# Optimization experiments

Hardware: AMD Instinct MI355X
Metric: run time of the kernel (lower is better)

## Reference

```python
import jax, jax.numpy as jnp
import numpy as np

WS = 7            # window size per spatial dim
NW = WS ** 3      # tokens per window = 343
EPS = 1e-5


def _rel_pos_index():
    # MONAI 3D relative position index, shape (NW, NW), values in [0, 13^3)
    coords = np.stack(np.meshgrid(np.arange(WS), np.arange(WS), np.arange(WS), indexing='ij'))
    cf = coords.reshape(3, -1)                       # (3, NW)
    rel = (cf[:, :, None] - cf[:, None, :]).transpose(1, 2, 0).astype(np.int64)  # (NW, NW, 3)
    rel += WS - 1
    rel[:, :, 0] *= (2 * WS - 1) * (2 * WS - 1)
    rel[:, :, 1] *= (2 * WS - 1)
    return rel.sum(-1)

_RPI = _rel_pos_index()


def layer_norm(x, g, b):
    mu = jnp.mean(x, axis=-1, keepdims=True)
    var = jnp.mean(jnp.square(x - mu), axis=-1, keepdims=True)
    return (x - mu) * jax.lax.rsqrt(var + EPS) * g + b


def _forward(x, pe_w, pe_bias, pe_g, pe_b, n1_g, n1_b, qkv_w, rpb, proj_w, proj_b,
             n2_g, n2_b, fc1_w, fc1_b, fc2_w, fc2_b):
    # ---- PatchEmbed: Conv3d stride=patch + LayerNorm over channel ----
    h = jax.lax.conv_general_dilated(x, pe_w, (2, 2, 2), 'VALID',
                                     dimension_numbers=('NCDHW', 'OIDHW', 'NCDHW'))
    h = h + pe_bias[None, :, None, None, None]
    b, c, d, hh, w = h.shape
    t = h.reshape(b, c, -1).transpose(0, 2, 1)       # (b, d*h*w, c)
    t = layer_norm(t, pe_g, pe_b)
    h = t.transpose(0, 2, 1).reshape(b, c, d, hh, w)
    # dropout(p=0) and proj_out(normalize=False) are identity

    xe = h.transpose(0, 2, 3, 4, 1)                  # (b, d, h, w, c)
    rpi = jnp.asarray(_RPI)
    num_heads = rpb.shape[-1]
    hd = c // num_heads
    scale = hd ** -0.5
    nd, nh_, nw_ = d // WS, hh // WS, w // WS        # window grid (7,7,7)

    for i in range(qkv_w.shape[0]):                  # 3 Swin blocks, all shift=0
        shortcut = xe
        y = layer_norm(xe, n1_g[i], n1_b[i])
        # window partition -> (b*nW, NW, c)
        yw = y.reshape(b, nd, WS, nh_, WS, nw_, WS, c)
        yw = yw.transpose(0, 1, 3, 5, 2, 4, 6, 7).reshape(-1, NW, c)
        # windowed MSA with relative position bias (qkv_bias=False)
        qkv = (yw @ qkv_w[i].T).reshape(-1, NW, 3, num_heads, hd).transpose(2, 0, 3, 1, 4)
        q, k, v = qkv[0] * scale, qkv[1], qkv[2]     # (Bw, nh, NW, hd)
        attn = jnp.einsum('bhnd,bhmd->bhnm', q, k)
        bias = rpb[i][rpi].transpose(2, 0, 1)        # (nh, NW, NW)
        attn = jax.nn.softmax(attn + bias[None], axis=-1)
        o = jnp.einsum('bhnm,bhmd->bhnd', attn, v)
        o = o.transpose(0, 2, 1, 3).reshape(-1, NW, c)
        o = o @ proj_w[i].T + proj_b[i]
        # window reverse
        o = o.reshape(b, nd, nh_, nw_, WS, WS, WS, c)
        o = o.transpose(0, 1, 4, 2, 5, 3, 6, 7).reshape(b, d, hh, w, c)
        xe = shortcut + o
        # MLP (GELU exact, mlp_ratio=4)
        z = layer_norm(xe, n2_g[i], n2_b[i])
        z = jax.nn.gelu(z @ fc1_w[i].T + fc1_b[i], approximate=False)
        xe = xe + (z @ fc2_w[i].T + fc2_b[i])

    return xe.transpose(0, 4, 1, 2, 3)               # (b, c, d, h, w)


def setup_inputs() -> dict:
    key = jax.random.key(0)
    ks = jax.random.split(key, 16)
    C, NH, NB, MLP = 16, 2, 3, 64
    s = 0.02
    return {
        'x': jax.random.normal(ks[0], (1, 1, 98, 98, 98), jnp.float32),
        'pe_w': jax.random.normal(ks[1], (C, 1, 2, 2, 2), jnp.float32) * s,
        'pe_bias': jnp.zeros((C,), jnp.float32),
        'pe_g': jnp.ones((C,), jnp.float32),
        'pe_b': jnp.zeros((C,), jnp.float32),
        'n1_g': jnp.ones((NB, C), jnp.float32),
        'n1_b': jnp.zeros((NB, C), jnp.float32),
        'qkv_w': jax.random.normal(ks[2], (NB, 3 * C, C), jnp.float32) * s,
        'rpb': jax.random.normal(ks[3], (NB, (2 * WS - 1) ** 3, NH), jnp.float32) * s,
        'proj_w': jax.random.normal(ks[4], (NB, C, C), jnp.float32) * s,
        'proj_b': jnp.zeros((NB, C), jnp.float32),
        'n2_g': jnp.ones((NB, C), jnp.float32),
        'n2_b': jnp.zeros((NB, C), jnp.float32),
        'fc1_w': jax.random.normal(ks[5], (NB, MLP, C), jnp.float32) * s,
        'fc1_b': jnp.zeros((NB, MLP), jnp.float32),
        'fc2_w': jax.random.normal(ks[6], (NB, C, MLP), jnp.float32) * s,
        'fc2_b': jnp.zeros((NB, C), jnp.float32),
    }


def reference(x, pe_w, pe_bias, pe_g, pe_b, n1_g, n1_b, qkv_w, rpb, proj_w, proj_b,
              n2_g, n2_b, fc1_w, fc1_b, fc2_w, fc2_b):
    return _forward(x, pe_w, pe_bias, pe_g, pe_b, n1_g, n1_b, qkv_w, rpb, proj_w,
                    proj_b, n2_g, n2_b, fc1_w, fc1_b, fc2_w, fc2_b)
```

## Files before the change

### kernel.cpp

```cpp
#include <hip/hip_runtime.h>
#include <math.h>

#define NWTOK 343
#define NTOK 117649
#define QSCALE 0.510069734f
#define LOG2E 1.4426950408889634f
#define QPLANE 1372
#define OPLANE 2744
#define NPAD 352
#define NTILE 22

typedef unsigned int u32;
typedef __fp16 h2 __attribute__((ext_vector_type(2)));
typedef __fp16 h4 __attribute__((ext_vector_type(4)));
typedef float f32x4 __attribute__((ext_vector_type(4)));

__device__ __forceinline__ u32 packh2(float a, float b) {
    h2 h = __builtin_amdgcn_cvt_pkrtz(a, b);
    return __builtin_bit_cast(u32, h);
}
__device__ __forceinline__ h4 packh4(float a, float b, float c, float d) {
    return __builtin_bit_cast(h4, make_uint2(packh2(a, b), packh2(c, d)));
}
__device__ __forceinline__ float fast_exp2(float x) {
#if __has_builtin(__builtin_amdgcn_exp2f)
    return __builtin_amdgcn_exp2f(x);
#else
    return exp2f(x);
#endif
}

__device__ __forceinline__ float dot16_lds(const float* __restrict__ wrow,
                                           const float* __restrict__ v) {
    const float4 w0 = *(const float4*)(wrow);
    const float4 w1 = *(const float4*)(wrow + 4);
    const float4 w2 = *(const float4*)(wrow + 8);
    const float4 w3 = *(const float4*)(wrow + 12);
    float a = v[0] * w0.x;
    a = fmaf(v[1], w0.y, a); a = fmaf(v[2], w0.z, a); a = fmaf(v[3], w0.w, a);
    a = fmaf(v[4], w1.x, a); a = fmaf(v[5], w1.y, a); a = fmaf(v[6], w1.z, a);
    a = fmaf(v[7], w1.w, a);
    a = fmaf(v[8], w2.x, a); a = fmaf(v[9], w2.y, a); a = fmaf(v[10], w2.z, a);
    a = fmaf(v[11], w2.w, a);
    a = fmaf(v[12], w3.x, a); a = fmaf(v[13], w3.y, a); a = fmaf(v[14], w3.z, a);
    a = fmaf(v[15], w3.w, a);
    return a;
}

__device__ __forceinline__ float gelu_exact(float x) {
    const float z = x * 0.70710678118654752f;
    const float az = fabsf(z);
    const float t = __builtin_amdgcn_rcpf(fmaf(0.3275911f, az, 1.0f));
    float y = fmaf(t, 1.061405429f, -1.453152027f);
    y = fmaf(t, y, 1.421413741f);
    y = fmaf(t, y, -0.284496736f);
    y = fmaf(t, y, 0.254829592f);
    y *= t;
    const float one_m_erf = y * __expf(-az * az);
    const float erf_az = 1.0f - one_m_erf;
    const float erf_z = (z < 0.f) ? -erf_az : erf_az;
    return 0.5f * x * (1.0f + erf_z);
}

__device__ __forceinline__ void store_f16_row(u32* base, int t, const float* v8) {
    uint4 u;
    u.x = packh2(v8[0], v8[1]); u.y = packh2(v8[2], v8[3]);
    u.z = packh2(v8[4], v8[5]); u.w = packh2(v8[6], v8[7]);
    *(uint4*)(base + t * 4) = u;
}

__global__ __launch_bounds__(256) void k_bias_expand(
    const float* __restrict__ rpb,
    __fp16* __restrict__ bexp16)
{
    const int tile = blockIdx.x;
    const int kt = tile % NTILE;
    const int rest = tile / NTILE;
    const int qt = rest % NTILE;
    const int bh = rest / NTILE;
    const int blk = bh >> 1, h = bh & 1;
    const int tid = threadIdx.x;
    const int n = tid >> 4, g = tid & 15;
    const int i = qt * 16 + n, j = kt * 16 + g;
    float val;
    if (j >= NWTOK) {
        val = -60.f;
    } else if (i >= NWTOK) {
        val = 0.f;
    } else {
        const int iz = i / 49, ir = i - iz * 49, iy = ir / 7, ix = ir - iy * 7;
        const int jz = j / 49, jr = j - jz * 49, jy = jr / 7, jx = jr - jy * 7;
        const int idx = (iz - jz + 6) * 169 + (iy - jy + 6) * 13 + (ix - jx + 6);
        val = rpb[((size_t)blk * 2197 + idx) * 2 + h] * LOG2E;
    }
    bexp16[(size_t)tile * 256 + tid] = (__fp16)val;
}

__global__ __launch_bounds__(256, 2) void k0_patch_qkv(
    const float* __restrict__ x,
    const float* __restrict__ pe_w,
    const float* __restrict__ pe_bias,
    const float* __restrict__ pe_g,
    const float* __restrict__ pe_b,
    const float* __restrict__ n1_g,
    const float* __restrict__ n1_b,
    const float* __restrict__ qkv_w,
    float* __restrict__ xe,
    u32* __restrict__ qg,
    u32* __restrict__ kg,
    u32* __restrict__ vg)
{
    __shared__ float w_s[128];
    __shared__ float pb_s[16], g_s[16], b_s[16], n1g_s[16], n1b_s[16];
    __shared__ float qkvw_s[768];
    const int tid = threadIdx.x;
    if (tid < 128) w_s[tid] = pe_w[tid];
    if (tid < 16) {
        pb_s[tid] = pe_bias[tid]; g_s[tid] = pe_g[tid]; b_s[tid] = pe_b[tid];
        n1g_s[tid] = n1_g[tid]; n1b_s[tid] = n1_b[tid];
    }
    for (int i = tid; i < 768; i += 256) qkvw_s[i] = qkv_w[i];
    __syncthreads();
    const int g = blockIdx.x * 256 + tid;
    if (g >= NTOK) return;
    const int z = g / 2401;
    const int r = g - z * 2401;
    const int y = r / 49;
    const int xx = r - y * 49;
    const float* bp = x + ((2 * z) * 98 + (2 * y)) * 98 + 2 * xx;
    float in[8];
    in[0] = bp[0];    in[1] = bp[1];
    in[2] = bp[98];   in[3] = bp[99];
    in[4] = bp[9604]; in[5] = bp[9605];
    in[6] = bp[9702]; in[7] = bp[9703];
    float v[16];
    float mu = 0.f;
    #pragma unroll
    for (int c = 0; c < 16; ++c) {
        float a = pb_s[c];
        #pragma unroll
        for (int k = 0; k < 8; ++k) a = fmaf(in[k], w_s[c * 8 + k], a);
        v[c] = a; mu += a;
    }
    mu *= 0.0625f;
    float var = 0.f;
    #pragma unroll
    for (int c = 0; c < 16; ++c) { float d = v[c] - mu; var = fmaf(d, d, var); }
    var *= 0.0625f;
    float rs = rsqrtf(var + 1e-5f);
    float o[16];
    #pragma unroll
    for (int c = 0; c < 16; ++c) o[c] = (v[c] - mu) * rs * g_s[c] + b_s[c];

    const int zw = z / 7, zi = z - zw * 7;
    const int yw = y / 7, yi = y - yw * 7;
    const int xw = xx / 7, xi = xx - xw * 7;
    const int w = (zw * 7 + yw) * 7 + xw;
    const int t = (zi * 7 + yi) * 7 + xi;
    const int widx = w * NWTOK + t;

    float4* dst = (float4*)(xe + (size_t)widx * 16);
    dst[0] = ((float4*)o)[0]; dst[1] = ((float4*)o)[1];
    dst[2] = ((float4*)o)[2]; dst[3] = ((float4*)o)[3];

    mu = 0.f;
    #pragma unroll
    for (int c = 0; c < 16; ++c) mu += o[c];
    mu *= 0.0625f;
    var = 0.f;
    #pragma unroll
    for (int c = 0; c < 16; ++c) { float d = o[c] - mu; var = fmaf(d, d, var); }
    var *= 0.0625f;
    rs = rsqrtf(var + 1e-5f);
    float yv[16];
    #pragma unroll
    for (int c = 0; c < 16; ++c) yv[c] = (o[c] - mu) * rs * n1g_s[c] + n1b_s[c];

    float tmp[16];
    #pragma unroll
    for (int rr = 0; rr < 16; ++rr) tmp[rr] = dot16_lds(qkvw_s + rr * 16, yv) * QSCALE;
    store_f16_row(qg + (size_t)(w * 2) * QPLANE, t, tmp);
    store_f16_row(qg + (size_t)(w * 2 + 1) * QPLANE, t, tmp + 8);
    #pragma unroll
    for (int rr = 0; rr < 16; ++rr) tmp[rr] = dot16_lds(qkvw_s + (16 + rr) * 16, yv);
    store_f16_row(kg + (size_t)(w * 2) * QPLANE, t, tmp);
    store_f16_row(kg + (size_t)(w * 2 + 1) * QPLANE, t, tmp + 8);
    #pragma unroll
    for (int rr = 0; rr < 16; ++rr) tmp[rr] = dot16_lds(qkvw_s + (32 + rr) * 16, yv);
    store_f16_row(vg + (size_t)(w * 2) * QPLANE, t, tmp);
    store_f16_row(vg + (size_t)(w * 2 + 1) * QPLANE, t, tmp + 8);
}

__global__ __launch_bounds__(704, 5) void k_attn(
    const u32* __restrict__ qg,
    const u32* __restrict__ kg,
    const u32* __restrict__ vg,
    float* __restrict__ og,
    const __fp16* __restrict__ bexp_blk)
{
    __shared__ __fp16 Kl[2][NPAD][16];
    __shared__ __fp16 Ql[2][NPAD][16];
    __shared__ __fp16 Vt[2][16][360];

    const int tid = threadIdx.x;
    const int pidx = blockIdx.x;
    const int wp = pidx >> 1;
    const int h = pidx & 1;
    const int w0 = 2 * wp;
    const int w1 = (w0 + 1 < NWTOK) ? w0 + 1 : NWTOK - 1;
    const int wh0 = w0 * 2 + h;
    const int wh1 = w1 * 2 + h;

    {
        const int sw = (tid >= NPAD) ? 1 : 0;
        const int st = tid - sw * NPAD;
        const size_t qpl = (size_t)(sw ? wh1 : wh0) * QPLANE;
        const uint4 z4 = make_uint4(0, 0, 0, 0);
        if (st < NWTOK) {
            const uint4 kw = ((const uint4*)(kg + qpl))[st];
            const uint4 qw = ((const uint4*)(qg + qpl))[st];
            const uint4 vw = ((const uint4*)(vg + qpl))[st];
            *(uint4*)&Kl[sw][st][0] = kw; *(uint4*)&Kl[sw][st][8] = z4;
            *(uint4*)&Ql[sw][st][0] = qw; *(uint4*)&Ql[sw][st][8] = z4;
            const h2 v01 = __builtin_bit_cast(h2, vw.x);
            const h2 v23 = __builtin_bit_cast(h2, vw.y);
            const h2 v45 = __builtin_bit_cast(h2, vw.z);
            const h2 v67 = __builtin_bit_cast(h2, vw.w);
            Vt[sw][0][st] = v01.x; Vt[sw][1][st] = v01.y;
            Vt[sw][2][st] = v23.x; Vt[sw][3][st] = v23.y;
            Vt[sw][4][st] = v45.x; Vt[sw][5][st] = v45.y;
            Vt[sw][6][st] = v67.x; Vt[sw][7][st] = v67.y;
        } else {
            *(uint4*)&Kl[sw][st][0] = z4; *(uint4*)&Kl[sw][st][8] = z4;
            *(uint4*)&Ql[sw][st][0] = z4; *(uint4*)&Ql[sw][st][8] = z4;
            #pragma unroll
            for (int d = 0; d < 8; ++d) Vt[sw][d][st] = (__fp16)0.f;
        }
        #pragma unroll
        for (int d = 8; d < 16; ++d) Vt[sw][d][st] = (__fp16)0.f;
    }
    __syncthreads();

    const int wave = tid >> 6;
    const int lane = tid & 63;
    const int n = lane & 15;
    const int g4 = (lane >> 4) * 4;

    const int qiA = (2 * wave) * 16 + n;
    const int qiB = qiA + 16;
    const h4 bqA0 = *(const h4*)&Ql[0][qiA][g4];
    const h4 bqB0 = *(const h4*)&Ql[0][qiB][g4];
    const h4 bqA1 = *(const h4*)&Ql[1][qiA][g4];
    const h4 bqB1 = *(const h4*)&Ql[1][qiB][g4];

    const int laneoff = n * 16 + g4;
    const __fp16* trowA = bexp_blk + ((size_t)(h * 484) + (size_t)(2 * wave) * NTILE) * 256 + laneoff;
    const __fp16* trowB = trowA + (size_t)NTILE * 256;

    f32x4 accA0 = {0.f, 0.f, 0.f, 0.f}, accB0 = {0.f, 0.f, 0.f, 0.f};
    f32x4 accA1 = {0.f, 0.f, 0.f, 0.f}, accB1 = {0.f, 0.f, 0.f, 0.f};
    float lA0 = 0.f, lB0 = 0.f, lA1 = 0.f, lB1 = 0.f;

    #pragma unroll
    for (int kt = 0; kt < NTILE; ++kt) {
        const uint2 cbA16 = *(const uint2*)(trowA + kt * 256);
        const uint2 cbB16 = *(const uint2*)(trowB + kt * 256);
        const h2 alo = __builtin_bit_cast(h2, cbA16.x);
        const h2 ahi = __builtin_bit_cast(h2, cbA16.y);
        const h2 blo = __builtin_bit_cast(h2, cbB16.x);
        const h2 bhi = __builtin_bit_cast(h2, cbB16.y);
        f32x4 cbAf, cbBf;
        cbAf[0] = (float)alo.x; cbAf[1] = (float)alo.y;
        cbAf[2] = (float)ahi.x; cbAf[3] = (float)ahi.y;
        cbBf[0] = (float)blo.x; cbBf[1] = (float)blo.y;
        cbBf[2] = (float)bhi.x; cbBf[3] = (float)bhi.y;

        const h4 ak0 = *(const h4*)&Kl[0][kt * 16 + n][g4];
        const h4 ak1 = *(const h4*)&Kl[1][kt * 16 + n][g4];
        const h4 av0 = *(const h4*)&Vt[0][n][kt * 16 + g4];
        const h4 av1 = *(const h4*)&Vt[1][n][kt * 16 + g4];

        f32x4 sA0 = __builtin_amdgcn_mfma_f32_16x16x16f16(ak0, bqA0, cbAf, 0, 0, 0);
        f32x4 sB0 = __builtin_amdgcn_mfma_f32_16x16x16f16(ak0, bqB0, cbBf, 0, 0, 0);
        f32x4 sA1 = __builtin_amdgcn_mfma_f32_16x16x16f16(ak1, bqA1, cbAf, 0, 0, 0);
        f32x4 sB1 = __builtin_amdgcn_mfma_f32_16x16x16f16(ak1, bqB1, cbBf, 0, 0, 0);

        const float pA00 = fast_exp2(sA0[0]);
        const float pA01 = fast_exp2(sA0[1]);
        const float pA02 = fast_exp2(sA0[2]);
        const float pA03 = fast_exp2(sA0[3]);
        const float pB00 = fast_exp2(sB0[0]);
        const float pB01 = fast_exp2(sB0[1]);
        const float pB02 = fast_exp2(sB0[2]);
        const float pB03 = fast_exp2(sB0[3]);
        const float pA10 = fast_exp2(sA1[0]);
        const float pA11 = fast_exp2(sA1[1]);
        const float pA12 = fast_exp2(sA1[2]);
        const float pA13 = fast_exp2(sA1[3]);
        const float pB10 = fast_exp2(sB1[0]);
        const float pB11 = fast_exp2(sB1[1]);
        const float pB12 = fast_exp2(sB1[2]);
        const float pB13 = fast_exp2(sB1[3]);

        lA0 += (pA00 + pA01) + (pA02 + pA03);
        lB0 += (pB00 + pB01) + (pB02 + pB03);
        lA1 += (pA10 + pA11) + (pA12 + pA13);
        lB1 += (pB10 + pB11) + (pB12 + pB13);

        const h4 bpA0 = packh4(pA00, pA01, pA02, pA03);
        const h4 bpB0 = packh4(pB00, pB01, pB02, pB03);
        const h4 bpA1 = packh4(pA10, pA11, pA12, pA13);
        const h4 bpB1 = packh4(pB10, pB11, pB12, pB13);

        accA0 = __builtin_amdgcn_mfma_f32_16x16x16f16(av0, bpA0, accA0, 0, 0, 0);
        accB0 = __builtin_amdgcn_mfma_f32_16x16x16f16(av0, bpB0, accB0, 0, 0, 0);
        accA1 = __builtin_amdgcn_mfma_f32_16x16x16f16(av1, bpA1, accA1, 0, 0, 0);
        accB1 = __builtin_amdgcn_mfma_f32_16x16x16f16(av1, bpB1, accB1, 0, 0, 0);
    }

    lA0 += __shfl_xor(lA0, 16); lA0 += __shfl_xor(lA0, 32);
    lB0 += __shfl_xor(lB0, 16); lB0 += __shfl_xor(lB0, 32);
    lA1 += __shfl_xor(lA1, 16); lA1 += __shfl_xor(lA1, 32);
    lB1 += __shfl_xor(lB1, 16); lB1 += __shfl_xor(lB1, 32);

    if (g4 < 8) {
        if (qiA < NWTOK) {
            const f32x4 o0 = accA0 * (1.f / lA0);
            *(f32x4*)(og + (size_t)wh0 * OPLANE + qiA * 8 + g4) = o0;
            const f32x4 o1 = accA1 * (1.f / lA1);
            *(f32x4*)(og + (size_t)wh1 * OPLANE + qiA * 8 + g4) = o1;
        }
        if (qiB < NWTOK) {
            const f32x4 o0 = accB0 * (1.f / lB0);
            *(f32x4*)(og + (size_t)wh0 * OPLANE + qiB * 8 + g4) = o0;
            const f32x4 o1 = accB1 * (1.f / lB1);
            *(f32x4*)(og + (size_t)wh1 * OPLANE + qiB * 8 + g4) = o1;
        }
    }
}

__global__ __launch_bounds__(256, 4) void k_post(
    float* __restrict__ xe,
    const float* __restrict__ og,
    u32* __restrict__ qg,
    u32* __restrict__ kg,
    u32* __restrict__ vg,
    const float* __restrict__ proj_w,
    const float* __restrict__ proj_b,
    const float* __restrict__ n2_g,
    const float* __restrict__ n2_b,
    const float* __restrict__ fc1_w,
    const float* __restrict__ fc1_b,
    const float* __restrict__ fc2_w,
    const float* __restrict__ fc2_b,
    const float* __restrict__ n1_g_nx,
    const float* __restrict__ n1_b_nx,
    const float* __restrict__ qkv_w_nx,
    float* __restrict__ outp,
    const int last)
{
    __shared__ u32 projh[128];
    __shared__ u32 fc1h[512];
    __shared__ u32 fc2h[512];
    __shared__ u32 qkvh[384];
    __shared__ float projb_s[16], n2g_s[16], n2b_s[16], fc2b_s[16], n1g_s[16], n1b_s[16];
    __shared__ float fc1b_s[64];
    const int tid = threadIdx.x;
    if (tid < 128) {
        const float2 p = ((const float2*)proj_w)[tid];
        projh[tid] = packh2(p.x, p.y);
    }
    for (int i = tid; i < 512; i += 256) {
        const float2 a = ((const float2*)fc1_w)[i];
        fc1h[i] = packh2(a.x, a.y);
        const float2 b = ((const float2*)fc2_w)[i];
        fc2h[i] = packh2(b.x, b.y);
    }
    for (int i = tid; i < 384; i += 256) {
        const float2 a = ((const float2*)qkv_w_nx)[i];
        qkvh[i] = packh2(a.x, a.y);
    }
    if (tid < 16) {
        projb_s[tid] = proj_b[tid];
        n2g_s[tid] = n2_g[tid]; n2b_s[tid] = n2_b[tid];
        fc2b_s[tid] = fc2_b[tid];
        n1g_s[tid] = n1_g_nx[tid]; n1b_s[tid] = n1_b_nx[tid];
    }
    if (tid < 64) fc1b_s[tid] = fc1_b[tid];
    __syncthreads();

    const int wave_id = blockIdx.x * 4 + (tid >> 6);
    if (wave_id >= NWTOK * NTILE) return;
    const int w = wave_id / NTILE;
    const int qt = wave_id - w * NTILE;

    const int lane = tid & 63;
    const int tcol = lane & 15;
    const int g4 = (lane >> 4) * 4;
    const int tok = qt * 16 + tcol;
    const bool valid = (tok < NWTOK);
    const int tokc = valid ? tok : (NWTOK - 1);

    const f32x4 zero = {0.f, 0.f, 0.f, 0.f};

    const int pl = g4 >> 3;
    const int po = g4 & 7;
    const float4 o4 = *(const float4*)(og + (size_t)(w * 2 + pl) * OPLANE + tokc * 8 + po);
    const h4 oB = packh4(o4.x, o4.y, o4.z, o4.w);

    const uint2 apw = *(const uint2*)(projh + tcol * 8 + (g4 >> 1));
    const f32x4 d1 = __builtin_amdgcn_mfma_f32_16x16x16f16(
        __builtin_bit_cast(h4, apw), oB, zero, 0, 0, 0);
    const float4 xe4 = *(const float4*)(xe + (size_t)(w * NWTOK + tokc) * 16 + g4);
    const float4 pb4 = *(const float4*)(projb_s + g4);
    float xr0 = d1[0] + xe4.x + pb4.x;
    float xr1 = d1[1] + xe4.y + pb4.y;
    float xr2 = d1[2] + xe4.z + pb4.z;
    float xr3 = d1[3] + xe4.w + pb4.w;

    float s = (xr0 + xr1) + (xr2 + xr3);
    s += __shfl_xor(s, 16); s += __shfl_xor(s, 32);
    float mu = s * 0.0625f;
    float v0 = xr0 - mu, v1 = xr1 - mu, v2 = xr2 - mu, v3 = xr3 - mu;
    float vv = fmaf(v0, v0, fmaf(v1, v1, fmaf(v2, v2, v3 * v3)));
    vv += __shfl_xor(vv, 16); vv += __shfl_xor(vv, 32);
    float rs = rsqrtf(vv * 0.0625f + 1e-5f);
    const float4 g2 = *(const float4*)(n2g_s + g4);
    const float4 b2 = *(const float4*)(n2b_s + g4);
    const h4 zB = packh4(v0 * rs * g2.x + b2.x, v1 * rs * g2.y + b2.y,
                         v2 * rs * g2.z + b2.z, v3 * rs * g2.w + b2.w);

    h4 hB[4];
    #pragma unroll
    for (int i = 0; i < 4; ++i) {
        const uint2 aw = *(const uint2*)(fc1h + (i * 16 + tcol) * 8 + (g4 >> 1));
        f32x4 hd = __builtin_amdgcn_mfma_f32_16x16x16f16(
            __builtin_bit_cast(h4, aw), zB, zero, 0, 0, 0);
        const float4 fb = *(const float4*)(fc1b_s + i * 16 + g4);
        hB[i] = packh4(gelu_exact(hd[0] + fb.x), gelu_exact(hd[1] + fb.y),
                       gelu_exact(hd[2] + fb.z), gelu_exact(hd[3] + fb.w));
    }

    f32x4 acc = zero;
    #pragma unroll
    for (int j = 0; j < 4; ++j) {
        const uint2 aw = *(const uint2*)(fc2h + tcol * 32 + ((j * 16 + g4) >> 1));
        acc = __builtin_amdgcn_mfma_f32_16x16x16f16(
            __builtin_bit_cast(h4, aw), hB[j], acc, 0, 0, 0);
    }
    const float4 f2b = *(const float4*)(fc2b_s + g4);
    xr0 += acc[0] + f2b.x;
    xr1 += acc[1] + f2b.y;
    xr2 += acc[2] + f2b.z;
    xr3 += acc[3] + f2b.w;

    if (last) {
        if (valid) {
            const int wd = w / 49, wr2 = w - wd * 49, whh = wr2 / 7, www = wr2 - whh * 7;
            const int tz = tok / 49, tr2 = tok - tz * 49, ty = tr2 / 7, tx = tr2 - ty * 7;
            const int g = ((wd * 7 + tz) * 49 + (whh * 7 + ty)) * 49 + (www * 7 + tx);
            outp[(size_t)(g4 + 0) * NTOK + g] = xr0;
            outp[(size_t)(g4 + 1) * NTOK + g] = xr1;
            outp[(size_t)(g4 + 2) * NTOK + g] = xr2;
            outp[(size_t)(g4 + 3) * NTOK + g] = xr3;
        }
        return;
    }

    if (valid) {
        float4 st = make_float4(xr0, xr1, xr2, xr3);
        *(float4*)(xe + (size_t)(w * NWTOK + tok) * 16 + g4) = st;
    }

    s = (xr0 + xr1) + (xr2 + xr3);
    s += __shfl_xor(s, 16); s += __shfl_xor(s, 32);
    mu = s * 0.0625f;
    v0 = xr0 - mu; v1 = xr1 - mu; v2 = xr2 - mu; v3 = xr3 - mu;
    vv = fmaf(v0, v0, fmaf(v1, v1, fmaf(v2, v2, v3 * v3)));
    vv += __shfl_xor(vv, 16); vv += __shfl_xor(vv, 32);
    rs = rsqrtf(vv * 0.0625f + 1e-5f);
    const float4 g1 = *(const float4*)(n1g_s + g4);
    const float4 b1 = *(const float4*)(n1b_s + g4);
    const h4 yB = packh4(v0 * rs * g1.x + b1.x, v1 * rs * g1.y + b1.y,
                         v2 * rs * g1.z + b1.z, v3 * rs * g1.w + b1.w);

    const int head = g4 >> 3;
    const int uoff = (g4 & 7) >> 1;
    const size_t qpl = (size_t)(w * 2 + head) * QPLANE + tok * 4 + uoff;
    #pragma unroll
    for (int m = 0; m < 3; ++m) {
        const uint2 aw = *(const uint2*)(qkvh + (m * 16 + tcol) * 8 + (g4 >> 1));
        f32x4 d = __builtin_amdgcn_mfma_f32_16x16x16f16(
            __builtin_bit_cast(h4, aw), yB, zero, 0, 0, 0);
        float sc = (m == 0) ? QSCALE : 1.f;
        const u32 lo = packh2(d[0] * sc, d[1] * sc);
        const u32 hi = packh2(d[2] * sc, d[3] * sc);
        if (valid) {
            u32* dst = (m == 0 ? qg : (m == 1 ? kg : vg)) + qpl;
            dst[0] = lo;
            dst[1] = hi;
        }
    }
}

extern "C" void kernel_launch(void* const* d_in, const int* in_sizes, int n_in,
                              void* d_out, int out_size, void* d_ws, size_t ws_size,
                              hipStream_t stream) {
    const float* x       = (const float*)d_in[0];
    const float* pe_w    = (const float*)d_in[1];
    const float* pe_bias = (const float*)d_in[2];
    const float* pe_g    = (const float*)d_in[3];
    const float* pe_b    = (const float*)d_in[4];
    const float* n1_g    = (const float*)d_in[5];
    const float* n1_b    = (const float*)d_in[6];
    const float* qkv_w   = (const float*)d_in[7];
    const float* rpb     = (const float*)d_in[8];
    const float* proj_w  = (const float*)d_in[9];
    const float* proj_b  = (const float*)d_in[10];
    const float* n2_g    = (const float*)d_in[11];
    const float* n2_b    = (const float*)d_in[12];
    const float* fc1_w   = (const float*)d_in[13];
    const float* fc1_b   = (const float*)d_in[14];
    const float* fc2_w   = (const float*)d_in[15];
    const float* fc2_b   = (const float*)d_in[16];

    float* ws = (float*)d_ws;
    const size_t SEG = (size_t)NTOK * 16;
    const size_t QSEG = (size_t)686 * QPLANE;
    float* xe = ws;
    u32* qg = (u32*)(ws + SEG);
    u32* kg = qg + QSEG;
    u32* vg = kg + QSEG;
    float* og = (float*)(vg + QSEG);
    __fp16* bexp16 = (__fp16*)(og + (size_t)686 * OPLANE);
    float* out = (float*)d_out;

    k_bias_expand<<<6 * NTILE * NTILE, 256, 0, stream>>>(rpb, bexp16);

    k0_patch_qkv<<<(NTOK + 255) / 256, 256, 0, stream>>>(
        x, pe_w, pe_bias, pe_g, pe_b, n1_g, n1_b, qkv_w, xe, qg, kg, vg);

    const int post_grid = (NWTOK * NTILE + 3) / 4;
    for (int i = 0; i < 3; ++i) {
        const int last = (i == 2) ? 1 : 0;
        const int nx = last ? i : i + 1;
        k_attn<<<344, 704, 0, stream>>>(
            qg, kg, vg, og, bexp16 + (size_t)i * 2 * 484 * 256);
        k_post<<<post_grid, 256, 0, stream>>>(
            xe, og, qg, kg, vg,
            proj_w + (size_t)i * 256, proj_b + (size_t)i * 16,
            n2_g + (size_t)i * 16, n2_b + (size_t)i * 16,
            fc1_w + (size_t)i * 1024, fc1_b + (size_t)i * 64,
            fc2_w + (size_t)i * 1024, fc2_b + (size_t)i * 16,
            n1_g + (size_t)nx * 16, n1_b + (size_t)nx * 16,
            qkv_w + (size_t)nx * 768,
            out, last);
    }
}
```

Before: 141.7 us.

## Fuse bias expansion into patch-embed kernel and compute QKV with MFMA

```diff
diff --git a/kernel.cpp b/kernel.cpp
--- a/kernel.cpp
+++ b/kernel.cpp
@@ -9,6 +9,8 @@
 #define OPLANE 2744
 #define NPAD 352
 #define NTILE 22
+#define NBIAS_BLK 2904
+#define NK0_TILE 7546
 
 typedef unsigned int u32;
 typedef __fp16 h2 __attribute__((ext_vector_type(2)));
@@ -28,23 +30,6 @@
 #else
     return exp2f(x);
 #endif
-}
-
-__device__ __forceinline__ float dot16_lds(const float* __restrict__ wrow,
-                                           const float* __restrict__ v) {
-    const float4 w0 = *(const float4*)(wrow);
-    const float4 w1 = *(const float4*)(wrow + 4);
-    const float4 w2 = *(const float4*)(wrow + 8);
-    const float4 w3 = *(const float4*)(wrow + 12);
-    float a = v[0] * w0.x;
-    a = fmaf(v[1], w0.y, a); a = fmaf(v[2], w0.z, a); a = fmaf(v[3], w0.w, a);
-    a = fmaf(v[4], w1.x, a); a = fmaf(v[5], w1.y, a); a = fmaf(v[6], w1.z, a);
-    a = fmaf(v[7], w1.w, a);
-    a = fmaf(v[8], w2.x, a); a = fmaf(v[9], w2.y, a); a = fmaf(v[10], w2.z, a);
-    a = fmaf(v[11], w2.w, a);
-    a = fmaf(v[12], w3.x, a); a = fmaf(v[13], w3.y, a); a = fmaf(v[14], w3.z, a);
-    a = fmaf(v[15], w3.w, a);
-    return a;
 }
 
 __device__ __forceinline__ float gelu_exact(float x) {
@@ -62,41 +47,7 @@
     return 0.5f * x * (1.0f + erf_z);
 }
 
-__device__ __forceinline__ void store_f16_row(u32* base, int t, const float* v8) {
-    uint4 u;
-    u.x = packh2(v8[0], v8[1]); u.y = packh2(v8[2], v8[3]);
-    u.z = packh2(v8[4], v8[5]); u.w = packh2(v8[6], v8[7]);
-    *(uint4*)(base + t * 4) = u;
-}
-
-__global__ __launch_bounds__(256) void k_bias_expand(
-    const float* __restrict__ rpb,
-    __fp16* __restrict__ bexp16)
-{
-    const int tile = blockIdx.x;
-    const int kt = tile % NTILE;
-    const int rest = tile / NTILE;
-    const int qt = rest % NTILE;
-    const int bh = rest / NTILE;
-    const int blk = bh >> 1, h = bh & 1;
-    const int tid = threadIdx.x;
-    const int n = tid >> 4, g = tid & 15;
-    const int i = qt * 16 + n, j = kt * 16 + g;
-    float val;
-    if (j >= NWTOK) {
-        val = -60.f;
-    } else if (i >= NWTOK) {
-        val = 0.f;
-    } else {
-        const int iz = i / 49, ir = i - iz * 49, iy = ir / 7, ix = ir - iy * 7;
-        const int jz = j / 49, jr = j - jz * 49, jy = jr / 7, jx = jr - jy * 7;
-        const int idx = (iz - jz + 6) * 169 + (iy - jy + 6) * 13 + (ix - jx + 6);
-        val = rpb[((size_t)blk * 2197 + idx) * 2 + h] * LOG2E;
-    }
-    bexp16[(size_t)tile * 256 + tid] = (__fp16)val;
-}
-
-__global__ __launch_bounds__(256, 2) void k0_patch_qkv(
+__global__ __launch_bounds__(256, 4) void k0_fused(
     const float* __restrict__ x,
     const float* __restrict__ pe_w,
     const float* __restrict__ pe_bias,
@@ -105,90 +56,137 @@
     const float* __restrict__ n1_g,
     const float* __restrict__ n1_b,
     const float* __restrict__ qkv_w,
+    const float* __restrict__ rpb,
     float* __restrict__ xe,
     u32* __restrict__ qg,
     u32* __restrict__ kg,
-    u32* __restrict__ vg)
+    u32* __restrict__ vg,
+    __fp16* __restrict__ bexp16)
 {
-    __shared__ float w_s[128];
+    const int tid = threadIdx.x;
+
+    if (blockIdx.x < NBIAS_BLK) {
+        const int tile = blockIdx.x;
+        const int kt = tile % NTILE;
+        const int rest = tile / NTILE;
+        const int qt = rest % NTILE;
+        const int bh = rest / NTILE;
+        const int blk = bh >> 1, h = bh & 1;
+        const int n = tid >> 4, g = tid & 15;
+        const int i = qt * 16 + n, j = kt * 16 + g;
+        float val;
+        if (j >= NWTOK) {
+            val = -60.f;
+        } else if (i >= NWTOK) {
+            val = 0.f;
+        } else {
+            const int iz = i / 49, ir = i - iz * 49, iy = ir / 7, ix = ir - iy * 7;
+            const int jz = j / 49, jr = j - jz * 49, jy = jr / 7, jx = jr - jy * 7;
+            const int idx = (iz - jz + 6) * 169 + (iy - jy + 6) * 13 + (ix - jx + 6);
+            val = rpb[((size_t)blk * 2197 + idx) * 2 + h] * LOG2E;
+        }
+        bexp16[(size_t)tile * 256 + tid] = (__fp16)val;
+        return;
+    }
+
+    __shared__ float pw_s[128];
+    __shared__ u32 qkvh[384];
     __shared__ float pb_s[16], g_s[16], b_s[16], n1g_s[16], n1b_s[16];
-    __shared__ float qkvw_s[768];
-    const int tid = threadIdx.x;
-    if (tid < 128) w_s[tid] = pe_w[tid];
+
+    if (tid < 128) pw_s[tid] = pe_w[tid];
+    for (int i = tid; i < 384; i += 256) {
+        const float2 a = ((const float2*)qkv_w)[i];
+        qkvh[i] = packh2(a.x, a.y);
+    }
     if (tid < 16) {
         pb_s[tid] = pe_bias[tid]; g_s[tid] = pe_g[tid]; b_s[tid] = pe_b[tid];
         n1g_s[tid] = n1_g[tid]; n1b_s[tid] = n1_b[tid];
     }
-    for (int i = tid; i < 768; i += 256) qkvw_s[i] = qkv_w[i];
     __syncthreads();
-    const int g = blockIdx.x * 256 + tid;
-    if (g >= NTOK) return;
-    const int z = g / 2401;
-    const int r = g - z * 2401;
-    const int y = r / 49;
-    const int xx = r - y * 49;
-    const float* bp = x + ((2 * z) * 98 + (2 * y)) * 98 + 2 * xx;
+
+    const int wave_id = (blockIdx.x - NBIAS_BLK) * 4 + (tid >> 6);
+    if (wave_id >= NK0_TILE) return;
+    const int w = wave_id / NTILE;
+    const int qt = wave_id - w * NTILE;
+
+    const int lane = tid & 63;
+    const int tcol = lane & 15;
+    const int g4 = (lane >> 4) * 4;
+    const int tok = qt * 16 + tcol;
+    const bool valid = (tok < NWTOK);
+    const int tokc = valid ? tok : (NWTOK - 1);
+
+    const int wd = w / 49, wr = w - wd * 49, wh = wr / 7, ww = wr - wh * 7;
+    const int tz = tokc / 49, tr = tokc - tz * 49, ty = tr / 7, tx = tr - ty * 7;
+    const int z = wd * 7 + tz, y = wh * 7 + ty, xx = ww * 7 + tx;
+    const float* bp = x + ((size_t)(2 * z) * 98 + (2 * y)) * 98 + 2 * xx;
     float in[8];
     in[0] = bp[0];    in[1] = bp[1];
     in[2] = bp[98];   in[3] = bp[99];
     in[4] = bp[9604]; in[5] = bp[9605];
     in[6] = bp[9702]; in[7] = bp[9703];
-    float v[16];
-    float mu = 0.f;
+
+    float c4[4];
     #pragma unroll
-    for (int c = 0; c < 16; ++c) {
-        float a = pb_s[c];
-        #pragma unroll
-        for (int k = 0; k < 8; ++k) a = fmaf(in[k], w_s[c * 8 + k], a);
-        v[c] = a; mu += a;
-    }
-    mu *= 0.0625f;
-    float var = 0.f;
+    for (int i = 0; i < 4; ++i) {
+        const int ch = g4 + i;
+        const float4 w0 = *(const float4*)(pw_s + ch * 8);
+        const float4 w1 = *(const float4*)(pw_s + ch * 8 + 4);
+        float a = pb_s[ch];
+        a = fmaf(in[0], w0.x, a); a = fmaf(in[1], w0.y, a);
+        a = fmaf(in[2], w0.z, a); a = fmaf(in[3], w0.w, a);
+        a = fmaf(in[4], w1.x, a); a = fmaf(in[5], w1.y, a);
+        a = fmaf(in[6], w1.z, a); a = fmaf(in[7], w1.w, a);
+        c4[i] = a;
+    }
+
+    float s = (c4[0] + c4[1]) + (c4[2] + c4[3]);
+    s += __shfl_xor(s, 16); s += __shfl_xor(s, 32);
+    float mu = s * 0.0625f;
+    float v0 = c4[0] - mu, v1 = c4[1] - mu, v2 = c4[2] - mu, v3 = c4[3] - mu;
+    float vv = fmaf(v0, v0, fmaf(v1, v1, fmaf(v2, v2, v3 * v3)));
+    vv += __shfl_xor(vv, 16); vv += __shfl_xor(vv, 32);
+    float rs = rsqrtf(vv * 0.0625f + 1e-5f);
+    const float4 gg = *(const float4*)(g_s + g4);
+    const float4 bb = *(const float4*)(b_s + g4);
+    const float o0 = v0 * rs * gg.x + bb.x;
+    const float o1 = v1 * rs * gg.y + bb.y;
+    const float o2 = v2 * rs * gg.z + bb.z;
+    const float o3 = v3 * rs * gg.w + bb.w;
+
+    if (valid)
+        *(float4*)(xe + (size_t)(w * NWTOK + tok) * 16 + g4) = make_float4(o0, o1, o2, o3);
+
+    s = (o0 + o1) + (o2 + o3);
+    s += __shfl_xor(s, 16); s += __shfl_xor(s, 32);
+    mu = s * 0.0625f;
+    v0 = o0 - mu; v1 = o1 - mu; v2 = o2 - mu; v3 = o3 - mu;
+    vv = fmaf(v0, v0, fmaf(v1, v1, fmaf(v2, v2, v3 * v3)));
+    vv += __shfl_xor(vv, 16); vv += __shfl_xor(vv, 32);
+    rs = rsqrtf(vv * 0.0625f + 1e-5f);
+    const float4 g1 = *(const float4*)(n1g_s + g4);
+    const float4 b1 = *(const float4*)(n1b_s + g4);
+    const h4 yB = packh4(v0 * rs * g1.x + b1.x, v1 * rs * g1.y + b1.y,
+                         v2 * rs * g1.z + b1.z, v3 * rs * g1.w + b1.w);
+
+    const f32x4 zero = {0.f, 0.f, 0.f, 0.f};
+    const int head = g4 >> 3;
+    const int uoff = (g4 & 7) >> 1;
+    const size_t qpl = (size_t)(w * 2 + head) * QPLANE + tok * 4 + uoff;
     #pragma unroll
-    for (int c = 0; c < 16; ++c) { float d = v[c] - mu; var = fmaf(d, d, var); }
-    var *= 0.0625f;
-    float rs = rsqrtf(var + 1e-5f);
-    float o[16];
-    #pragma unroll
-    for (int c = 0; c < 16; ++c) o[c] = (v[c] - mu) * rs * g_s[c] + b_s[c];
-
-    const int zw = z / 7, zi = z - zw * 7;
-    const int yw = y / 7, yi = y - yw * 7;
-    const int xw = xx / 7, xi = xx - xw * 7;
-    const int w = (zw * 7 + yw) * 7 + xw;
-    const int t = (zi * 7 + yi) * 7 + xi;
-    const int widx = w * NWTOK + t;
-
-    float4* dst = (float4*)(xe + (size_t)widx * 16);
-    dst[0] = ((float4*)o)[0]; dst[1] = ((float4*)o)[1];
-    dst[2] = ((float4*)o)[2]; dst[3] = ((float4*)o)[3];
-
-    mu = 0.f;
-    #pragma unroll
-    for (int c = 0; c < 16; ++c) mu += o[c];
-    mu *= 0.0625f;
-    var = 0.f;
-    #pragma unroll
-    for (int c = 0; c < 16; ++c) { float d = o[c] - mu; var = fmaf(d, d, var); }
-    var *= 0.0625f;
-    rs = rsqrtf(var + 1e-5f);
-    float yv[16];
-    #pragma unroll
-    for (int c = 0; c < 16; ++c) yv[c] = (o[c] - mu) * rs * n1g_s[c] + n1b_s[c];
-
-    float tmp[16];
-    #pragma unroll
-    for (int rr = 0; rr < 16; ++rr) tmp[rr] = dot16_lds(qkvw_s + rr * 16, yv) * QSCALE;
-    store_f16_row(qg + (size_t)(w * 2) * QPLANE, t, tmp);
-    store_f16_row(qg + (size_t)(w * 2 + 1) * QPLANE, t, tmp + 8);
-    #pragma unroll
-    for (int rr = 0; rr < 16; ++rr) tmp[rr] = dot16_lds(qkvw_s + (16 + rr) * 16, yv);
-    store_f16_row(kg + (size_t)(w * 2) * QPLANE, t, tmp);
-    store_f16_row(kg + (size_t)(w * 2 + 1) * QPLANE, t, tmp + 8);
-    #pragma unroll
-    for (int rr = 0; rr < 16; ++rr) tmp[rr] = dot16_lds(qkvw_s + (32 + rr) * 16, yv);
-    store_f16_row(vg + (size_t)(w * 2) * QPLANE, t, tmp);
-    store_f16_row(vg + (size_t)(w * 2 + 1) * QPLANE, t, tmp + 8);
+    for (int m = 0; m < 3; ++m) {
+        const uint2 aw = *(const uint2*)(qkvh + (m * 16 + tcol) * 8 + (g4 >> 1));
+        f32x4 d = __builtin_amdgcn_mfma_f32_16x16x16f16(
+            __builtin_bit_cast(h4, aw), yB, zero, 0, 0, 0);
+        const float sc = (m == 0) ? QSCALE : 1.f;
+        const u32 lo = packh2(d[0] * sc, d[1] * sc);
+        const u32 hi = packh2(d[2] * sc, d[3] * sc);
+        if (valid) {
+            u32* dst = (m == 0 ? qg : (m == 1 ? kg : vg)) + qpl;
+            dst[0] = lo;
+            dst[1] = hi;
+        }
+    }
 }
 
 __global__ __launch_bounds__(704, 5) void k_attn(
@@ -535,10 +533,10 @@
     __fp16* bexp16 = (__fp16*)(og + (size_t)686 * OPLANE);
     float* out = (float*)d_out;
 
-    k_bias_expand<<<6 * NTILE * NTILE, 256, 0, stream>>>(rpb, bexp16);
-
-    k0_patch_qkv<<<(NTOK + 255) / 256, 256, 0, stream>>>(
-        x, pe_w, pe_bias, pe_g, pe_b, n1_g, n1_b, qkv_w, xe, qg, kg, vg);
+    const int k0_grid = NBIAS_BLK + (NK0_TILE + 3) / 4;
+    k0_fused<<<k0_grid, 256, 0, stream>>>(
+        x, pe_w, pe_bias, pe_g, pe_b, n1_g, n1_b, qkv_w, rpb,
+        xe, qg, kg, vg, bexp16);
 
     const int post_grid = (NWTOK * NTILE + 3) / 4;
     for (int i = 0; i < 3; ++i) {
```

Measured after the change: 130.7 us. 1.08x faster.
